# Kernel optimization log

Measured on AMD Instinct MI355X. Metric: run time of the kernel, lower is better.

The kernel has to match this reference:

```python
import jax, jax.numpy as jnp
import numpy as np

DIM = 512
HEADS = 8
HD = DIM // HEADS
HIDDEN = 4 * DIM
EPS = 1e-5


def layernorm(x, g, b):
    mu = jnp.mean(x, axis=-1, keepdims=True)
    var = jnp.mean(jnp.square(x - mu), axis=-1, keepdims=True)
    return (x - mu) * jax.lax.rsqrt(var + EPS) * g + b


def setup_inputs() -> dict:
    key = jax.random.key(0)
    ks = jax.random.split(key, 10)
    B, P, N, C = 16, 4, 256, DIM
    s = 1.0 / np.sqrt(C)
    sh = 1.0 / np.sqrt(HIDDEN)
    return {
        "x": jax.random.normal(ks[0], (B, P, N, C), jnp.float32),
        "ln1_g": jnp.ones((C,), jnp.float32),
        "ln1_b": jnp.zeros((C,), jnp.float32),
        "w_qkv": jax.random.uniform(ks[1], (3 * C, C), jnp.float32, -s, s),
        "w_proj": jax.random.uniform(ks[2], (C, C), jnp.float32, -s, s),
        "b_proj": jax.random.uniform(ks[3], (C,), jnp.float32, -s, s),
        "ln2_g": jnp.ones((C,), jnp.float32),
        "ln2_b": jnp.zeros((C,), jnp.float32),
        "w1": jax.random.uniform(ks[4], (HIDDEN, C), jnp.float32, -s, s),
        "b1": jax.random.uniform(ks[5], (HIDDEN,), jnp.float32, -s, s),
        "w2": jax.random.uniform(ks[6], (C, HIDDEN), jnp.float32, -sh, sh),
        "b2": jax.random.uniform(ks[7], (C,), jnp.float32, -sh, sh),
    }


def reference(x, ln1_g, ln1_b, w_qkv, w_proj, b_proj, ln2_g, ln2_b, w1, b1, w2, b2):
    B, P, N, C = x.shape
    # --- attention branch (batched over B, P, heads; same math as the unrolled loops) ---
    h = layernorm(x, ln1_g, ln1_b)
    qkv = jnp.einsum('bpnc,dc->bpnd', h, w_qkv)            # [B,P,N,3C]
    qkv = qkv.reshape(B, P, N, 3, HEADS, HD)
    q, k, v = qkv[..., 0, :, :], qkv[..., 1, :, :], qkv[..., 2, :, :]  # [B,P,N,H,hd]
    scale = HD ** -0.5
    attn = jnp.einsum('bpnhd,bpmhd->bphnm', q * scale, k)  # [B,P,H,N,N]
    attn = jax.nn.softmax(attn, axis=-1)
    o = jnp.einsum('bphnm,bpmhd->bpnhd', attn, v).reshape(B, P, N, C)
    o = jnp.einsum('bpnc,dc->bpnd', o, w_proj) + b_proj
    x = x + o
    # --- MLP branch ---
    h = layernorm(x, ln2_g, ln2_b)
    h = jax.nn.gelu(jnp.einsum('bpnc,hc->bpnh', h, w1) + b1, approximate=False)
    h = jnp.einsum('bpnh,ch->bpnc', h, w2) + b2
    return x + h
```

## Files before the change

### kernel.cpp

```cpp
#include <hip/hip_runtime.h>

typedef __attribute__((ext_vector_type(8))) short short8;
typedef __attribute__((ext_vector_type(4))) float f32x4;
typedef __attribute__((ext_vector_type(4))) unsigned short u16x4;
typedef __attribute__((ext_vector_type(2))) unsigned int u32x2;
typedef __attribute__((ext_vector_type(4))) unsigned int u32x4;

__device__ __forceinline__ float bf2f(unsigned short u) {
    return __uint_as_float(((unsigned)u) << 16);
}
__device__ __forceinline__ unsigned short f2bf(float f) {
    unsigned u = __float_as_uint(f);
    u += 0x7fffu + ((u >> 16) & 1u);
    return (unsigned short)(u >> 16);
}
__device__ __forceinline__ unsigned pack2(float a, float b) {
    unsigned r;
    asm("v_cvt_pk_bf16_f32 %0, %1, %2" : "=v"(r) : "v"(a), "v"(b));
    return r;
}
__device__ __forceinline__ void load_lds16(const void* g, void* l) {
    __builtin_amdgcn_global_load_lds(
        (const __attribute__((address_space(1))) void*)g,
        (__attribute__((address_space(3))) void*)l, 16, 0, 0);
}
__device__ __forceinline__ bool is_bf16(const unsigned* dt) {
    return *dt == 0x3F803F80u;
}
__device__ __forceinline__ float gelu_fast(float t) {
    float q = t * (1.5957691f + 0.07135482f * t * t);
    float e = __expf(-q);
    return __fdividef(t, 1.0f + e);
}

__global__ __launch_bounds__(512) void cast_all(
    const void* s_wqkv, const void* s_wproj, const void* s_w1, const void* s_w2,
    const void* v0, const void* v1, const void* v2, const void* v3,
    const void* v4, const void* v5, const void* v6,
    unsigned short* d_wqkv, unsigned short* d_wproj, unsigned short* d_w1,
    unsigned short* d_w2, unsigned short* par, const unsigned* dt)
{
    bool isbf = is_bf16(dt);
    int b = blockIdx.x, tid = threadIdx.x;
    if (b < 768) {
        const void* src; unsigned short* dst; int off;
        if (b < 192)      { src = s_wqkv;  dst = d_wqkv;  off = b * 4096; }
        else if (b < 256) { src = s_wproj; dst = d_wproj; off = (b - 192) * 4096; }
        else if (b < 512) { src = s_w1;    dst = d_w1;    off = (b - 256) * 4096; }
        else              { src = s_w2;    dst = d_w2;    off = (b - 512) * 4096; }
        int i = off + tid * 8;
        if (isbf) {
            *(short8*)(dst + i) = *(const short8*)((const unsigned short*)src + i);
        } else {
            const float* s = (const float*)src + i;
            short8 o;
            #pragma unroll
            for (int j = 0; j < 8; ++j) o[j] = (short)f2bf(s[j]);
            *(short8*)(dst + i) = o;
        }
    } else {
        const void* srcs[7]  = {v0, v1, v2, v3, v4, v5, v6};
        const int   sizes[7] = {512, 512, 512, 512, 512, 2048, 512};
        const int   offs[7]  = {0, 512, 1024, 1536, 2048, 2560, 4608};
        int j = b - 768;
        const void* s = srcs[j];
        unsigned short* d = par + offs[j];
        for (int i = tid; i < sizes[j]; i += 512)
            d[i] = isbf ? ((const unsigned short*)s)[i] : f2bf(((const float*)s)[i]);
    }
}

__global__ __launch_bounds__(256) void ln_kernel(
    const void* __restrict__ xin, size_t row0,
    const unsigned* __restrict__ dt, int inmode,
    const unsigned short* __restrict__ g, const unsigned short* __restrict__ b,
    unsigned short* __restrict__ y)
{
    int w = threadIdx.x >> 6, lane = threadIdx.x & 63;
    size_t lr = (size_t)blockIdx.x * 4 + w;
    size_t gr = row0 + lr;
    bool isf32 = (inmode == 1) || (inmode == 0 && !is_bf16(dt));
    float v[8];
    if (isf32) {
        const float* xr = (const float*)xin + (gr << 9) + (lane << 3);
        #pragma unroll
        for (int j = 0; j < 8; ++j) v[j] = xr[j];
    } else {
        short8 raw = *(const short8*)((const unsigned short*)xin + (gr << 9) + (lane << 3));
        #pragma unroll
        for (int j = 0; j < 8; ++j) v[j] = bf2f((unsigned short)raw[j]);
    }
    float sum = 0.f, sq = 0.f;
    #pragma unroll
    for (int j = 0; j < 8; ++j) { sum += v[j]; sq += v[j] * v[j]; }
    #pragma unroll
    for (int off = 32; off > 0; off >>= 1) {
        sum += __shfl_xor(sum, off);
        sq  += __shfl_xor(sq, off);
    }
    float mu  = sum * (1.0f / 512.0f);
    float var = sq * (1.0f / 512.0f) - mu * mu;
    float rs  = rsqrtf(var + 1e-5f);
    short8 gr8 = *(const short8*)(g + (lane << 3));
    short8 br8 = *(const short8*)(b + (lane << 3));
    float o[8];
    #pragma unroll
    for (int j = 0; j < 8; ++j)
        o[j] = (v[j] - mu) * rs * bf2f((unsigned short)gr8[j]) + bf2f((unsigned short)br8[j]);
    u32x4 ov = {pack2(o[0], o[1]), pack2(o[2], o[3]),
                pack2(o[4], o[5]), pack2(o[6], o[7])};
    *(u32x4*)(y + (lr << 9) + (lane << 3)) = ov;
}

__global__ __launch_bounds__(256, 2) void gemm_big(
    const unsigned short* __restrict__ A, const unsigned short* __restrict__ W,
    const unsigned short* __restrict__ bias,
    unsigned short* __restrict__ out,
    int NBY, int N, int K, int mode)
{
    __shared__ char lds[49152];

    int tid = threadIdx.x;
    int w = tid >> 6, lane = tid & 63;
    int l15 = lane & 15, g = lane >> 4;

    int L = blockIdx.x;
    int bx, by;
    if ((NBY & 7) == 0) {
        int nby8 = NBY >> 3;
        int xcd = L & 7, i = L >> 3;
        by = xcd * nby8 + (i % nby8);
        bx = i / nby8;
    } else {
        by = L % NBY;
        bx = L / NBY;
    }
    int m0 = by << 8, n0 = bx << 7;
    int wm = (w >> 1) << 7;
    int wn = (w & 1) << 6;

    int srow = tid >> 3;
    int u = (tid & 7) ^ (srow & 7);
    const unsigned short* gA[8];
    const unsigned short* gB[4];
    #pragma unroll
    for (int j = 0; j < 8; ++j)
        gA[j] = A + (size_t)(m0 + j * 32 + srow) * K + u * 8;
    #pragma unroll
    for (int j = 0; j < 4; ++j)
        gB[j] = W + (size_t)(n0 + j * 32 + srow) * K + u * 8;
    int lslot = tid * 16;
    int swz = l15 & 7;

    f32x4 acc[4][8];
    #pragma unroll
    for (int i = 0; i < 4; ++i)
        #pragma unroll
        for (int j = 0; j < 8; ++j) acc[i][j] = (f32x4){0.f, 0.f, 0.f, 0.f};

    for (int k = 0; k < K; k += 64) {
        if (k > 0) __syncthreads();
        #pragma unroll
        for (int j = 0; j < 8; ++j)
            load_lds16(gA[j] + k, &lds[j * 4096 + lslot]);
        #pragma unroll
        for (int j = 0; j < 4; ++j)
            load_lds16(gB[j] + k, &lds[32768 + j * 4096 + lslot]);
        __syncthreads();
        const char* bAct = lds;
        const char* bW = lds + 32768;
        #pragma unroll
        for (int s = 0; s < 2; ++s) {
            int cs = ((s * 4 + g) ^ swz) << 4;
            short8 wf[4];
            #pragma unroll
            for (int i = 0; i < 4; ++i)
                wf[i] = *(const short8*)(bW + (wn + i * 16 + l15) * 128 + cs);
            #pragma unroll
            for (int jg = 0; jg < 8; jg += 4) {
                short8 af[4];
                #pragma unroll
                for (int j = 0; j < 4; ++j)
                    af[j] = *(const short8*)(bAct + (wm + (jg + j) * 16 + l15) * 128 + cs);
                #pragma unroll
                for (int i = 0; i < 4; ++i)
                    #pragma unroll
                    for (int j = 0; j < 4; ++j)
                        acc[i][jg + j] = __builtin_amdgcn_mfma_f32_16x16x32_bf16(
                            wf[i], af[j], acc[i][jg + j], 0, 0, 0);
            }
        }
    }
    __syncthreads();

    if (mode == 2) {
        #pragma unroll
        for (int i = 0; i < 4; ++i) {
            u16x4 bb = *(const u16x4*)(bias + n0 + wn + i * 16 + g * 4);
            #pragma unroll
            for (int j = 0; j < 8; ++j)
                #pragma unroll
                for (int r = 0; r < 4; ++r)
                    acc[i][j][r] = gelu_fast(acc[i][j][r] + bf2f(bb[r]));
        }
    }

    #pragma unroll
    for (int hh = 0; hh < 2; ++hh) {
        if ((w >> 1) == hh) {
            #pragma unroll
            for (int j = 0; j < 8; ++j) {
                int mloc = j * 16 + l15;
                char* rowp = lds + mloc * 256;
                int sw = mloc & 30;
                #pragma unroll
                for (int i = 0; i < 4; ++i) {
                    int cq = (wn + i * 16 + g * 4) >> 2;
                    u32x2 pk = {pack2(acc[i][j][0], acc[i][j][1]),
                                pack2(acc[i][j][2], acc[i][j][3])};
                    *(u32x2*)(rowp + ((cq ^ sw) << 3)) = pk;
                }
            }
        }
        __syncthreads();
        int rL = tid >> 4, lc = tid & 15;
        int colg = n0 + lc * 8;
        #pragma unroll
        for (int ps = 0; ps < 8; ++ps) {
            int row = ps * 16 + rL;
            int rowL = m0 + hh * 128 + row;
            int c16 = lc ^ ((row >> 1) & 15);
            short8 vv = *(const short8*)(lds + row * 256 + (c16 << 4));
            *(short8*)(out + (size_t)rowL * N + colg) = vv;
        }
        if (hh == 0) __syncthreads();
    }
}

__global__ __launch_bounds__(256) void gemm8(
    const unsigned short* __restrict__ A, const unsigned short* __restrict__ W,
    const unsigned short* __restrict__ bias,
    const void* __restrict__ resid, size_t rrow0,
    void* __restrict__ out, size_t orow0,
    int NBY, int N, int K, int mode, const unsigned* __restrict__ dt)
{
    constexpr int BN = 128;
    __shared__ char lds[32768];

    int tid = threadIdx.x;
    int w = tid >> 6, lane = tid & 63;
    int l15 = lane & 15, g = lane >> 4;

    int L = blockIdx.x;
    int bx, by;
    if ((NBY & 7) == 0) {
        int nby8 = NBY >> 3;
        int xcd = L & 7, i = L >> 3;
        by = xcd * nby8 + (i % nby8);
        bx = i / nby8;
    } else {
        by = L % NBY;
        bx = L / NBY;
    }
    int m0 = by << 7, n0 = bx << 7;
    int wm = (w >> 1) << 6;
    int wn = (w & 1) << 6;

    int srow_t = tid >> 3;
    int u_t = (tid & 7) ^ (srow_t & 7);
    const unsigned short* gA[4];
    const unsigned short* gB[4];
    #pragma unroll
    for (int j = 0; j < 4; ++j) {
        gA[j] = A + (size_t)(m0 + j * 32 + srow_t) * K + u_t * 8;
        gB[j] = W + (size_t)(n0 + j * 32 + srow_t) * K + u_t * 8;
    }
    int lslot = tid * 16;
    int swz = l15 & 7;

    f32x4 acc[4][4];
    #pragma unroll
    for (int i = 0; i < 4; ++i)
        #pragma unroll
        for (int j = 0; j < 4; ++j) acc[i][j] = (f32x4){0.f, 0.f, 0.f, 0.f};

    for (int k = 0; k < K; k += 64) {
        if (k > 0) __syncthreads();
        #pragma unroll
        for (int j = 0; j < 4; ++j) {
            load_lds16(gA[j] + k, &lds[j * 4096 + lslot]);
            load_lds16(gB[j] + k, &lds[16384 + j * 4096 + lslot]);
        }
        __syncthreads();
        const char* bAct = lds;
        const char* bW = bAct + 16384;
        #pragma unroll
        for (int s = 0; s < 2; ++s) {
            int cs = ((s * 4 + g) ^ swz) << 4;
            short8 wf[4], af[4];
            #pragma unroll
            for (int i = 0; i < 4; ++i)
                wf[i] = *(const short8*)(bW + (wn + i * 16 + l15) * 128 + cs);
            #pragma unroll
            for (int j = 0; j < 4; ++j)
                af[j] = *(const short8*)(bAct + (wm + j * 16 + l15) * 128 + cs);
            #pragma unroll
            for (int i = 0; i < 4; ++i)
                #pragma unroll
                for (int j = 0; j < 4; ++j)
                    acc[i][j] = __builtin_amdgcn_mfma_f32_16x16x32_bf16(wf[i], af[j], acc[i][j], 0, 0, 0);
        }
    }
    __syncthreads();

    if (mode == 2) {
        #pragma unroll
        for (int i = 0; i < 4; ++i) {
            u16x4 bb = *(const u16x4*)(bias + n0 + wn + i * 16 + g * 4);
            #pragma unroll
            for (int j = 0; j < 4; ++j)
                #pragma unroll
                for (int r = 0; r < 4; ++r)
                    acc[i][j][r] = gelu_fast(acc[i][j][r] + bf2f(bb[r]));
        }
    }

    char* tb = (char*)lds;
    #pragma unroll
    for (int j = 0; j < 4; ++j) {
        int mloc = wm + j * 16 + l15;
        char* rowp = tb + mloc * (BN * 2);
        int sw = mloc & (BN / 4 - 2);
        #pragma unroll
        for (int i = 0; i < 4; ++i) {
            int cq = (wn + i * 16 + g * 4) >> 2;
            u32x2 pk = {pack2(acc[i][j][0], acc[i][j][1]),
                        pack2(acc[i][j][2], acc[i][j][3])};
            *(u32x2*)(rowp + ((cq ^ sw) << 3)) = pk;
        }
    }
    __syncthreads();

    int rL = tid >> 4;
    int lc = tid & 15;
    bool inbf = is_bf16(dt);
    int colg = n0 + lc * 8;
    float bv[8];
    if (mode == 1 || mode == 3) {
        short8 bb = *(const short8*)(bias + colg);
        #pragma unroll
        for (int t = 0; t < 8; ++t) bv[t] = bf2f((unsigned short)bb[t]);
    }

    #pragma unroll
    for (int ps = 0; ps < 8; ++ps) {
        int row = ps * 16 + rL;
        int rowL = m0 + row;
        int c16 = lc ^ ((row >> 1) & 15);
        short8 vv = *(const short8*)(tb + row * (BN * 2) + (c16 << 4));

        if (mode == 0 || mode == 2) {
            *(short8*)((unsigned short*)out + (size_t)rowL * N + colg) = vv;
        } else if (mode == 1) {
            size_t rbase = (rrow0 + rowL) * (size_t)N + colg;
            float o8[8];
            if (inbf) {
                short8 rr = *(const short8*)((const unsigned short*)resid + rbase);
                #pragma unroll
                for (int t = 0; t < 8; ++t)
                    o8[t] = bf2f((unsigned short)rr[t]) + bf2f((unsigned short)vv[t]) + bv[t];
            } else {
                f32x4 r0 = *(const f32x4*)((const float*)resid + rbase);
                f32x4 r1 = *(const f32x4*)((const float*)resid + rbase + 4);
                #pragma unroll
                for (int t = 0; t < 4; ++t) {
                    o8[t]     = r0[t] + bf2f((unsigned short)vv[t]) + bv[t];
                    o8[t + 4] = r1[t] + bf2f((unsigned short)vv[t + 4]) + bv[t + 4];
                }
            }
            u32x4 ov = {pack2(o8[0], o8[1]), pack2(o8[2], o8[3]),
                        pack2(o8[4], o8[5]), pack2(o8[6], o8[7])};
            *(u32x4*)((unsigned short*)out + (size_t)rowL * N + colg) = ov;
        } else {
            size_t rbase = (size_t)rowL * N + colg;
            short8 rr = *(const short8*)((const unsigned short*)resid + rbase);
            float o8[8];
            #pragma unroll
            for (int t = 0; t < 8; ++t)
                o8[t] = bf2f((unsigned short)rr[t]) + bf2f((unsigned short)vv[t]) + bv[t];
            size_t obase = (orow0 + rowL) * (size_t)N + colg;
            if (inbf) {
                u32x4 ov = {pack2(o8[0], o8[1]), pack2(o8[2], o8[3]),
                            pack2(o8[4], o8[5]), pack2(o8[6], o8[7])};
                *(u32x4*)((unsigned short*)out + obase) = ov;
            } else {
                float* ob = (float*)out + obase;
                *(f32x4*)ob       = (f32x4){o8[0], o8[1], o8[2], o8[3]};
                *(f32x4*)(ob + 4) = (f32x4){o8[4], o8[5], o8[6], o8[7]};
            }
        }
    }
}

__global__ __launch_bounds__(256) void attn_mfma(
    const unsigned short* __restrict__ qkv, unsigned short* __restrict__ o)
{
    __shared__ unsigned short Vt[64 * 256];
    __shared__ unsigned short Ps[4][16 * 256];
    int bp = blockIdx.x >> 3, h = blockIdx.x & 7;
    const unsigned short* base = qkv + (size_t)bp * 256 * 1536;
    int qo = h << 6, ko = 512 + (h << 6), vo = 1024 + (h << 6);
    int tid = threadIdx.x, w = tid >> 6, lane = tid & 63;
    int l15 = lane & 15, g = lane >> 4;

    {
        int d = tid & 63;
        for (int s = tid >> 6; s < 256; s += 4) {
            unsigned short v = base[(size_t)s * 1536 + vo + d];
            *(unsigned short*)((char*)Vt + d * 512 + (((s >> 3) ^ (d & 7)) << 4) + ((s & 7) << 1)) = v;
        }
    }
    __syncthreads();

    unsigned short* P = Ps[w];

    for (int pass = 0; pass < 4; ++pass) {
        int q0 = pass * 64 + w * 16;
        short8 qa[2];
        #pragma unroll
        for (int t = 0; t < 2; ++t)
            qa[t] = *(const short8*)(base + (size_t)(q0 + l15) * 1536 + qo + t * 32 + g * 8);
        f32x4 S[16];
        #pragma unroll
        for (int ns = 0; ns < 16; ++ns) {
            f32x4 a = {0.f, 0.f, 0.f, 0.f};
            #pragma unroll
            for (int t = 0; t < 2; ++t) {
                short8 kb = *(const short8*)(base + (size_t)(ns * 16 + l15) * 1536 + ko + t * 32 + g * 8);
                a = __builtin_amdgcn_mfma_f32_16x16x32_bf16(qa[t], kb, a, 0, 0, 0);
            }
            S[ns] = a;
        }
        float mx[4], sums[4], inv[4];
        #pragma unroll
        for (int r = 0; r < 4; ++r) {
            float m = -1e30f;
            #pragma unroll
            for (int ns = 0; ns < 16; ++ns) m = fmaxf(m, S[ns][r]);
            m *= 0.125f;
            #pragma unroll
            for (int off = 1; off < 16; off <<= 1) m = fmaxf(m, __shfl_xor(m, off));
            mx[r] = m;
            sums[r] = 0.f;
        }
        #pragma unroll
        for (int ns = 0; ns < 16; ++ns)
            #pragma unroll
            for (int r = 0; r < 4; ++r) {
                float p = __expf(S[ns][r] * 0.125f - mx[r]);
                sums[r] += p;
                S[ns][r] = p;
            }
        #pragma unroll
        for (int r = 0; r < 4; ++r) {
            float s2 = sums[r];
            #pragma unroll
            for (int off = 1; off < 16; off <<= 1) s2 += __shfl_xor(s2, off);
            inv[r] = 1.0f / s2;
        }
        #pragma unroll
        for (int ns = 0; ns < 16; ++ns)
            #pragma unroll
            for (int r = 0; r < 4; ++r) {
                int mq = g * 4 + r;
                int s = ns * 16 + l15;
                *(unsigned short*)((char*)P + mq * 512 + (((s >> 3) ^ (mq & 7)) << 4) + ((s & 7) << 1))
                    = f2bf(S[ns][r] * inv[r]);
            }
        f32x4 O[4];
        #pragma unroll
        for (int ds = 0; ds < 4; ++ds) O[ds] = (f32x4){0.f, 0.f, 0.f, 0.f};
        #pragma unroll
        for (int ks = 0; ks < 8; ++ks) {
            int c = (ks * 4 + g) ^ (l15 & 7);
            short8 pa = *(const short8*)((const char*)P + l15 * 512 + (c << 4));
            #pragma unroll
            for (int ds = 0; ds < 4; ++ds) {
                short8 vb = *(const short8*)((const char*)Vt + (ds * 16 + l15) * 512 + (c << 4));
                O[ds] = __builtin_amdgcn_mfma_f32_16x16x32_bf16(pa, vb, O[ds], 0, 0, 0);
            }
        }
        #pragma unroll
        for (int ds = 0; ds < 4; ++ds)
            #pragma unroll
            for (int r = 0; r < 4; ++r) {
                int mq = q0 + g * 4 + r;
                int d = ds * 16 + l15;
                o[((size_t)(bp * 256 + mq) << 9) + (h << 6) + d] = f2bf(O[ds][r]);
            }
    }
}

extern "C" void kernel_launch(void* const* d_in, const int* in_sizes, int n_in,
                              void* d_out, int out_size, void* d_ws, size_t ws_size,
                              hipStream_t stream)
{
    const void* x      = d_in[0];
    const void* ln1_g  = d_in[1];
    const void* ln1_b  = d_in[2];
    const void* w_qkv  = d_in[3];
    const void* w_proj = d_in[4];
    const void* b_proj = d_in[5];
    const void* ln2_g  = d_in[6];
    const void* ln2_b  = d_in[7];
    const void* w1     = d_in[8];
    const void* b1     = d_in[9];
    const void* w2     = d_in[10];
    const void* b2     = d_in[11];
    const unsigned* dt = (const unsigned*)ln1_g;

    const int M = 16384;
    char* ws = (char*)d_ws;
    unsigned short* wqkv_b  = (unsigned short*)(ws);
    unsigned short* wproj_b = (unsigned short*)(ws + 1572864);
    unsigned short* w1_b    = (unsigned short*)(ws + 2097152);
    unsigned short* w2_b    = (unsigned short*)(ws + 4194304);
    unsigned short* par     = (unsigned short*)(ws + 6291456);
    const size_t CAST_END = 6308096;

    unsigned short* p_g1    = par + 0;
    unsigned short* p_b1ln  = par + 512;
    unsigned short* p_bproj = par + 1024;
    unsigned short* p_g2    = par + 1536;
    unsigned short* p_b2ln  = par + 2048;
    unsigned short* p_b1    = par + 2560;
    unsigned short* p_b2    = par + 4608;

    int NC = 64;
    const int cand[7] = {1, 2, 4, 8, 16, 32, 64};
    for (int i = 0; i < 7; ++i) {
        size_t need = CAST_END + (size_t)(M / cand[i]) * 10240;
        if (need <= ws_size) { NC = cand[i]; break; }
    }
    const int R = M / NC;

    char* cb = ws + CAST_END;
    unsigned short* h   = (unsigned short*)(cb);
    unsigned short* qkv = (unsigned short*)(cb + (size_t)R * 1024);
    unsigned short* o   = (unsigned short*)(cb + (size_t)R * 4096);
    unsigned short* x2  = (unsigned short*)(cb + (size_t)R * 5120);
    unsigned short* hid = (unsigned short*)(cb + (size_t)R * 6144);
    unsigned short* h2  = h;

    cast_all<<<775, 512, 0, stream>>>(w_qkv, w_proj, w1, w2,
                                      ln1_g, ln1_b, b_proj, ln2_g, ln2_b, b1, b2,
                                      wqkv_b, wproj_b, w1_b, w2_b, par, dt);

    for (int c = 0; c < NC; ++c) {
        const size_t r0 = (size_t)c * R;
        const int NBY  = R / 128;
        const int NBY2 = R / 256;

        ln_kernel<<<R / 4, 256, 0, stream>>>(x, r0, dt, 0, p_g1, p_b1ln, h);
        gemm_big<<<(1536 / 128) * NBY2, 256, 0, stream>>>(
            h, wqkv_b, nullptr, qkv, NBY2, 1536, 512, 0);
        attn_mfma<<<(R / 256) * 8, 256, 0, stream>>>(qkv, o);
        gemm8<<<(512 / 128) * NBY, 256, 0, stream>>>(
            o, wproj_b, p_bproj, x, r0, x2, 0, NBY, 512, 512, 1, dt);
        ln_kernel<<<R / 4, 256, 0, stream>>>(x2, 0, dt, 2, p_g2, p_b2ln, h2);
        gemm_big<<<(2048 / 128) * NBY2, 256, 0, stream>>>(
            h2, w1_b, p_b1, hid, NBY2, 2048, 512, 2);
        gemm8<<<(512 / 128) * NBY, 256, 0, stream>>>(
            hid, w2_b, p_b2, x2, 0, d_out, r0, NBY, 512, 2048, 3, dt);
    }
}
```

Before: 312.5 us.

## Skip weight cast for bf16 inputs, write gemm_big output directly from registers

The input dtype is now detected on the host from the input size, so the weight/param cast kernel is skipped and raw bf16 weights are used directly when inputs are already bf16. The dtype flag is passed as a kernel argument instead of being read from device memory in each kernel. gemm_big's epilogue no longer stages output through LDS with barriers and writes packed 8-byte fragments straight to global memory, trading coalescing for fewer syncs. Dead mode branches are removed from gemm8. With the default fp32 inputs the cast still runs, so the main effect is the epilogue change.

```diff
diff --git a/kernel.cpp b/kernel.cpp
--- a/kernel.cpp
+++ b/kernel.cpp
@@ -71,15 +71,13 @@
 }
 
 __global__ __launch_bounds__(256) void ln_kernel(
-    const void* __restrict__ xin, size_t row0,
-    const unsigned* __restrict__ dt, int inmode,
+    const void* __restrict__ xin, size_t row0, int isf32,
     const unsigned short* __restrict__ g, const unsigned short* __restrict__ b,
     unsigned short* __restrict__ y)
 {
     int w = threadIdx.x >> 6, lane = threadIdx.x & 63;
     size_t lr = (size_t)blockIdx.x * 4 + w;
     size_t gr = row0 + lr;
-    bool isf32 = (inmode == 1) || (inmode == 0 && !is_bf16(dt));
     float v[8];
     if (isf32) {
         const float* xr = (const float*)xin + (gr << 9) + (lane << 3);
@@ -191,7 +189,6 @@
             }
         }
     }
-    __syncthreads();
 
     if (mode == 2) {
         #pragma unroll
@@ -205,35 +202,16 @@
         }
     }
 
-    #pragma unroll
-    for (int hh = 0; hh < 2; ++hh) {
-        if ((w >> 1) == hh) {
-            #pragma unroll
-            for (int j = 0; j < 8; ++j) {
-                int mloc = j * 16 + l15;
-                char* rowp = lds + mloc * 256;
-                int sw = mloc & 30;
-                #pragma unroll
-                for (int i = 0; i < 4; ++i) {
-                    int cq = (wn + i * 16 + g * 4) >> 2;
-                    u32x2 pk = {pack2(acc[i][j][0], acc[i][j][1]),
-                                pack2(acc[i][j][2], acc[i][j][3])};
-                    *(u32x2*)(rowp + ((cq ^ sw) << 3)) = pk;
-                }
-            }
-        }
-        __syncthreads();
-        int rL = tid >> 4, lc = tid & 15;
-        int colg = n0 + lc * 8;
-        #pragma unroll
-        for (int ps = 0; ps < 8; ++ps) {
-            int row = ps * 16 + rL;
-            int rowL = m0 + hh * 128 + row;
-            int c16 = lc ^ ((row >> 1) & 15);
-            short8 vv = *(const short8*)(lds + row * 256 + (c16 << 4));
-            *(short8*)(out + (size_t)rowL * N + colg) = vv;
-        }
-        if (hh == 0) __syncthreads();
+    unsigned short* ob = out + (size_t)(m0 + wm + l15) * N + (n0 + wn + (g << 2));
+    #pragma unroll
+    for (int j = 0; j < 8; ++j) {
+        unsigned short* orow = ob + (size_t)(j * 16) * N;
+        #pragma unroll
+        for (int i = 0; i < 4; ++i) {
+            u32x2 pk = {pack2(acc[i][j][0], acc[i][j][1]),
+                        pack2(acc[i][j][2], acc[i][j][3])};
+            *(u32x2*)(orow + i * 16) = pk;
+        }
     }
 }
 
@@ -242,7 +220,7 @@
     const unsigned short* __restrict__ bias,
     const void* __restrict__ resid, size_t rrow0,
     void* __restrict__ out, size_t orow0,
-    int NBY, int N, int K, int mode, const unsigned* __restrict__ dt)
+    int NBY, int N, int K, int mode, int inbf)
 {
     constexpr int BN = 128;
     __shared__ char lds[32768];
@@ -313,18 +291,6 @@
     }
     __syncthreads();
 
-    if (mode == 2) {
-        #pragma unroll
-        for (int i = 0; i < 4; ++i) {
-            u16x4 bb = *(const u16x4*)(bias + n0 + wn + i * 16 + g * 4);
-            #pragma unroll
-            for (int j = 0; j < 4; ++j)
-                #pragma unroll
-                for (int r = 0; r < 4; ++r)
-                    acc[i][j][r] = gelu_fast(acc[i][j][r] + bf2f(bb[r]));
-        }
-    }
-
     char* tb = (char*)lds;
     #pragma unroll
     for (int j = 0; j < 4; ++j) {
@@ -343,10 +309,9 @@
 
     int rL = tid >> 4;
     int lc = tid & 15;
-    bool inbf = is_bf16(dt);
     int colg = n0 + lc * 8;
     float bv[8];
-    if (mode == 1 || mode == 3) {
+    {
         short8 bb = *(const short8*)(bias + colg);
         #pragma unroll
         for (int t = 0; t < 8; ++t) bv[t] = bf2f((unsigned short)bb[t]);
@@ -359,9 +324,7 @@
         int c16 = lc ^ ((row >> 1) & 15);
         short8 vv = *(const short8*)(tb + row * (BN * 2) + (c16 << 4));
 
-        if (mode == 0 || mode == 2) {
-            *(short8*)((unsigned short*)out + (size_t)rowL * N + colg) = vv;
-        } else if (mode == 1) {
+        if (mode == 1) {
             size_t rbase = (rrow0 + rowL) * (size_t)N + colg;
             float o8[8];
             if (inbf) {
@@ -519,6 +482,8 @@
     const void* b2     = d_in[11];
     const unsigned* dt = (const unsigned*)ln1_g;
 
+    const int isbf = (in_sizes[1] == 512 * 2);
+
     const int M = 16384;
     char* ws = (char*)d_ws;
     unsigned short* wqkv_b  = (unsigned short*)(ws);
@@ -528,13 +493,17 @@
     unsigned short* par     = (unsigned short*)(ws + 6291456);
     const size_t CAST_END = 6308096;
 
-    unsigned short* p_g1    = par + 0;
-    unsigned short* p_b1ln  = par + 512;
-    unsigned short* p_bproj = par + 1024;
-    unsigned short* p_g2    = par + 1536;
-    unsigned short* p_b2ln  = par + 2048;
-    unsigned short* p_b1    = par + 2560;
-    unsigned short* p_b2    = par + 4608;
+    const unsigned short* p_wqkv  = isbf ? (const unsigned short*)w_qkv  : wqkv_b;
+    const unsigned short* p_wproj = isbf ? (const unsigned short*)w_proj : wproj_b;
+    const unsigned short* p_w1    = isbf ? (const unsigned short*)w1     : w1_b;
+    const unsigned short* p_w2    = isbf ? (const unsigned short*)w2     : w2_b;
+    const unsigned short* p_g1    = isbf ? (const unsigned short*)ln1_g  : par + 0;
+    const unsigned short* p_b1ln  = isbf ? (const unsigned short*)ln1_b  : par + 512;
+    const unsigned short* p_bproj = isbf ? (const unsigned short*)b_proj : par + 1024;
+    const unsigned short* p_g2    = isbf ? (const unsigned short*)ln2_g  : par + 1536;
+    const unsigned short* p_b2ln  = isbf ? (const unsigned short*)ln2_b  : par + 2048;
+    const unsigned short* p_b1    = isbf ? (const unsigned short*)b1     : par + 2560;
+    const unsigned short* p_b2    = isbf ? (const unsigned short*)b2     : par + 4608;
 
     int NC = 64;
     const int cand[7] = {1, 2, 4, 8, 16, 32, 64};
@@ -552,25 +521,27 @@
     unsigned short* hid = (unsigned short*)(cb + (size_t)R * 6144);
     unsigned short* h2  = h;
 
-    cast_all<<<775, 512, 0, stream>>>(w_qkv, w_proj, w1, w2,
-                                      ln1_g, ln1_b, b_proj, ln2_g, ln2_b, b1, b2,
-                                      wqkv_b, wproj_b, w1_b, w2_b, par, dt);
+    if (!isbf) {
+        cast_all<<<775, 512, 0, stream>>>(w_qkv, w_proj, w1, w2,
+                                          ln1_g, ln1_b, b_proj, ln2_g, ln2_b, b1, b2,
+                                          wqkv_b, wproj_b, w1_b, w2_b, par, dt);
+    }
 
     for (int c = 0; c < NC; ++c) {
         const size_t r0 = (size_t)c * R;
         const int NBY  = R / 128;
         const int NBY2 = R / 256;
 
-        ln_kernel<<<R / 4, 256, 0, stream>>>(x, r0, dt, 0, p_g1, p_b1ln, h);
+        ln_kernel<<<R / 4, 256, 0, stream>>>(x, r0, isbf ? 0 : 1, p_g1, p_b1ln, h);
         gemm_big<<<(1536 / 128) * NBY2, 256, 0, stream>>>(
-            h, wqkv_b, nullptr, qkv, NBY2, 1536, 512, 0);
+            h, p_wqkv, nullptr, qkv, NBY2, 1536, 512, 0);
         attn_mfma<<<(R / 256) * 8, 256, 0, stream>>>(qkv, o);
         gemm8<<<(512 / 128) * NBY, 256, 0, stream>>>(
-            o, wproj_b, p_bproj, x, r0, x2, 0, NBY, 512, 512, 1, dt);
-        ln_kernel<<<R / 4, 256, 0, stream>>>(x2, 0, dt, 2, p_g2, p_b2ln, h2);
+            o, p_wproj, p_bproj, x, r0, x2, 0, NBY, 512, 512, 1, isbf);
+        ln_kernel<<<R / 4, 256, 0, stream>>>(x2, 0, 0, p_g2, p_b2ln, h2);
         gemm_big<<<(2048 / 128) * NBY2, 256, 0, stream>>>(
-            h2, w1_b, p_b1, hid, NBY2, 2048, 512, 2);
+            h2, p_w1, p_b1, hid, NBY2, 2048, 512, 2);
         gemm8<<<(512 / 128) * NBY, 256, 0, stream>>>(
-            hid, w2_b, p_b2, x2, 0, d_out, r0, NBY, 512, 2048, 3, dt);
-    }
-}
+            hid, p_w2, p_b2, x2, 0, d_out, r0, NBY, 512, 2048, 3, isbf);
+    }
+}
```

After: 321.8 us. +3.0%, slower.
